# Kernel tuning notes

Hardware: AMD Instinct MI355X
Metric: run time of the kernel (lower is better)

## Reference

```python
import jax, jax.numpy as jnp
import numpy as np

B, L, C, H, W = 2, 3, 64, 32, 32
DI, N, DT_RANK, K = 128, 16, 4, 4  # d_inner=2*C, d_state, dt_rank=ceil(C/16), 4 scan dirs


def setup_inputs() -> dict:
    key = jax.random.key(0)
    ks = iter(jax.random.split(key, 48))
    nrm = lambda shape, s=0.02: jax.random.normal(next(ks), shape, jnp.float32) * s
    return {
        "image_sequence": jax.random.normal(next(ks), (B, L, C, H, W), jnp.float32),
        "difficult_zone": jax.random.normal(next(ks), (B, C, H, W), jnp.float32),
        "sigma": jax.random.uniform(next(ks), (B, C, H, W), jnp.float32),
        # LayerNorm2d applied to each frame
        "norm_g": jnp.ones((C,)), "norm_b": jnp.zeros((C,)),
        # ConvolutionalResBlock (in=3C -> out=C), GroupNorm(num_groups=1)
        "gn1_g": jnp.ones((3 * C,)), "gn1_b": jnp.zeros((3 * C,)),
        "conv1_w": nrm((C, 3 * C, 3, 3)), "conv1_b": jnp.zeros((C,)),
        "gn2_g": jnp.ones((C,)), "gn2_b": jnp.zeros((C,)),
        "conv2_w": nrm((C, C, 3, 3)), "conv2_b": jnp.zeros((C,)),
        "skip_w": nrm((C, 3 * C, 1, 1)), "skip_b": jnp.zeros((C,)),
        # VSSBlock pre-norms
        "ln1_g": jnp.ones((C,)), "ln1_b": jnp.zeros((C,)),
        "ln2_g": jnp.ones((C,)), "ln2_b": jnp.zeros((C,)),
        # SS2D
        "in_proj_w": nrm((2 * DI, C)),
        "dwconv_w": nrm((DI, 1, 3, 3)), "dwconv_b": jnp.zeros((DI,)),
        "x_proj_w": nrm((K, DT_RANK + 2 * N, DI)),
        "dt_proj_w": nrm((K, DI, DT_RANK), 0.1),
        "dt_proj_b": jnp.log(jnp.expm1(jnp.full((K, DI), 0.01, jnp.float32))),
        "A_logs": jnp.log(jnp.tile(jnp.arange(1, N + 1, dtype=jnp.float32), (K * DI, 1))),
        "Ds": jnp.ones((K * DI,)),
        "out_norm_g": jnp.ones((DI,)), "out_norm_b": jnp.zeros((DI,)),
        "out_proj_w": nrm((C, DI)),
        # Mlp (hidden = C)
        "fc1_w": nrm((C, C)), "fc1_b": jnp.zeros((C,)),
        "fc2_w": nrm((C, C)), "fc2_b": jnp.zeros((C,)),
    }


def _ln(x, g, b, eps=1e-5):  # layernorm over last axis
    m = x.mean(-1, keepdims=True)
    v = x.var(-1, keepdims=True)
    return (x - m) * jax.lax.rsqrt(v + eps) * g + b


def _ln2d(x, g, b, eps=1e-6):  # per-pixel channel layernorm, NCHW
    m = x.mean(1, keepdims=True)
    v = x.var(1, keepdims=True)
    return (x - m) * jax.lax.rsqrt(v + eps) * g[None, :, None, None] + b[None, :, None, None]


def _gn1(x, g, b, eps=1e-5):  # GroupNorm(num_groups=1), NCHW
    m = x.mean((1, 2, 3), keepdims=True)
    v = x.var((1, 2, 3), keepdims=True)
    return (x - m) * jax.lax.rsqrt(v + eps) * g[None, :, None, None] + b[None, :, None, None]


def _conv(x, w, b, pad):
    y = jax.lax.conv_general_dilated(x, w, (1, 1), [(pad, pad), (pad, pad)],
                                     dimension_numbers=("NCHW", "OIHW", "NCHW"))
    return y + b[None, :, None, None]


def _forward(image_sequence, difficult_zone, sigma, norm_g, norm_b, gn1_g, gn1_b,
             conv1_w, conv1_b, gn2_g, gn2_b, conv2_w, conv2_b, skip_w, skip_b,
             ln1_g, ln1_b, ln2_g, ln2_b, in_proj_w, dwconv_w, dwconv_b, x_proj_w,
             dt_proj_w, dt_proj_b, A_logs, Ds, out_norm_g, out_norm_b, out_proj_w,
             fc1_w, fc1_b, fc2_w, fc2_b):
    b, l, c, h, w = image_sequence.shape
    bl, L2 = b * l, h * w
    # fold frame loop into batch (identical math per frame in the torch loop)
    frames = _ln2d(image_sequence.reshape(bl, c, h, w), norm_g, norm_b)
    dz = jnp.broadcast_to(difficult_zone[:, None], (b, l, c, h, w)).reshape(bl, c, h, w)
    sg = jnp.broadcast_to(sigma[:, None], (b, l, c, h, w)).reshape(bl, c, h, w)
    x = jnp.concatenate([dz, frames, sg], axis=1)  # [bl, 3c, h, w]
    # channel compressor: pre-act conv res block
    hdn = _conv(jax.nn.silu(_gn1(x, gn1_g, gn1_b)), conv1_w, conv1_b, 1)
    hdn = _conv(jax.nn.silu(_gn1(hdn, gn2_g, gn2_b)), conv2_w, conv2_b, 1)
    x = hdn + _conv(x, skip_w, skip_b, 0)          # [bl, c, h, w]
    x = x.transpose(0, 2, 3, 1)                    # [bl, h, w, c]
    # --- VSSBlock (pre-norm): x = x + SS2D(LN(x)) ---
    xn = _ln(x, ln1_g, ln1_b)
    xz = xn @ in_proj_w.T                          # [bl,h,w,2*DI]
    xc, z = jnp.split(xz, 2, axis=-1)
    xc = xc.transpose(0, 3, 1, 2)                  # [bl, DI, h, w]
    xc = jax.lax.conv_general_dilated(xc, dwconv_w, (1, 1), [(1, 1), (1, 1)],
                                      dimension_numbers=("NCHW", "OIHW", "NCHW"),
                                      feature_group_count=DI) + dwconv_b[None, :, None, None]
    xc = jax.nn.silu(xc)
    # 4-direction scan inputs (HW, WH, and their reverses)
    xf = xc.reshape(bl, DI, L2)
    xt = xc.transpose(0, 1, 3, 2).reshape(bl, DI, L2)
    xs = jnp.stack([xf, xt], axis=1)
    xs = jnp.concatenate([xs, jnp.flip(xs, axis=-1)], axis=1)  # [bl, 4, DI, L2]
    x_dbl = jnp.einsum("bkdl,kcd->bkcl", xs, x_proj_w)
    dts, Bs, Cs = jnp.split(x_dbl, [DT_RANK, DT_RANK + N], axis=2)
    dts = jnp.einsum("bkrl,kdr->bkdl", dts, dt_proj_w) + dt_proj_b[None, :, :, None]
    dts = jax.nn.softplus(dts)                     # [bl, 4, DI, L2]
    A = -jnp.exp(A_logs).reshape(K, DI, N)
    dA = jnp.exp(dts[..., None] * A[None, :, :, None, :])            # [bl,4,DI,L2,N]
    dBu = dts[..., None] * Bs.transpose(0, 1, 3, 2)[:, :, None] * xs[..., None]
    a_t = dA.transpose(3, 0, 1, 2, 4)              # [L2, bl, 4, DI, N]
    bu_t = dBu.transpose(3, 0, 1, 2, 4)
    c_t = Cs.transpose(3, 0, 1, 2)                 # [L2, bl, 4, N]

    def step(hid, inp):
        a_i, bu_i, c_i = inp
        hid = a_i * hid + bu_i
        return hid, jnp.einsum("bkdn,bkn->bkd", hid, c_i)

    h0 = jnp.zeros((bl, K, DI, N), xs.dtype)
    _, ys = jax.lax.scan(step, h0, (a_t, bu_t, c_t))                 # [L2, bl, 4, DI]
    ys = ys.transpose(1, 2, 3, 0) + xs * Ds.reshape(K, DI)[None, :, :, None]
    inv = jnp.flip(ys[:, 2:4], axis=-1)
    y = (ys[:, 0] + inv[:, 0]
         + ys[:, 1].reshape(bl, DI, w, h).transpose(0, 1, 3, 2).reshape(bl, DI, L2)
         + inv[:, 1].reshape(bl, DI, w, h).transpose(0, 1, 3, 2).reshape(bl, DI, L2))
    y = _ln(y.transpose(0, 2, 1), out_norm_g, out_norm_b).reshape(bl, h, w, DI)
    y = y * jax.nn.silu(z)
    x = x + y @ out_proj_w.T
    # --- x = x + Mlp(LN(x)) ---
    xn = _ln(x, ln2_g, ln2_b)
    x = x + (jax.nn.gelu(xn @ fc1_w.T + fc1_b, approximate=False) @ fc2_w.T + fc2_b)
    return x.transpose(0, 3, 1, 2).reshape(b, l, c, h, w)


def reference(image_sequence, difficult_zone, sigma, norm_g, norm_b, gn1_g, gn1_b,
              conv1_w, conv1_b, gn2_g, gn2_b, conv2_w, conv2_b, skip_w, skip_b,
              ln1_g, ln1_b, ln2_g, ln2_b, in_proj_w, dwconv_w, dwconv_b, x_proj_w,
              dt_proj_w, dt_proj_b, A_logs, Ds, out_norm_g, out_norm_b, out_proj_w,
              fc1_w, fc1_b, fc2_w, fc2_b):
    return _forward(image_sequence, difficult_zone, sigma, norm_g, norm_b, gn1_g, gn1_b,
                    conv1_w, conv1_b, gn2_g, gn2_b, conv2_w, conv2_b, skip_w, skip_b,
                    ln1_g, ln1_b, ln2_g, ln2_b, in_proj_w, dwconv_w, dwconv_b, x_proj_w,
                    dt_proj_w, dt_proj_b, A_logs, Ds, out_norm_g, out_norm_b, out_proj_w,
                    fc1_w, fc1_b, fc2_w, fc2_b)
```

## Files before the change

### kernel.cpp

```cpp
#include <hip/hip_runtime.h>
#include <math.h>

#define BL    6
#define CCH   64
#define C3    192
#define L2    1024
#define DIC   128
#define NST   16
#define K4    4
#define PSTR  1088
#define NCH   32

#define LOG2E 1.44269504088896340736f
#define LN2C  0.69314718055994530942f

__device__ __forceinline__ float fexp(float x){ return __builtin_amdgcn_exp2f(x*LOG2E); }
__device__ __forceinline__ float fsilu(float x){ return x * __builtin_amdgcn_rcpf(1.f + fexp(-x)); }
__device__ __forceinline__ float fsoftplus(float x){
  if (x > 20.f) return x;
  return __builtin_amdgcn_logf(1.f + fexp(x)) * LN2C;
}
__device__ __forceinline__ float fgelu(float x){
  return 0.5f*x*(1.f + erff(x*0.70710678118654752440f));
}

__global__ __launch_bounds__(256) void k_ln2d(const float* __restrict__ img,
    const float* __restrict__ dz, const float* __restrict__ sg,
    const float* __restrict__ g, const float* __restrict__ b, float* __restrict__ x3c,
    float* __restrict__ psum1, float* __restrict__ psq1){
  __shared__ float ps[4][8], pq[4][8], gs[4], gq[4];
  int s = blockIdx.x >> 7;
  int pg = blockIdx.x & 127;
  int tid = threadIdx.x;
  int px = tid & 7; int cg = tid >> 3;
  int wv = tid >> 6; int lane = tid & 63;
  int p = pg*8 + px;
  int bsmp = s/3;
  const float* fr = img + (size_t)s*CCH*L2;
  float vals[2]; float sm=0.f, sq=0.f;
  #pragma unroll
  for (int j=0;j<2;++j){
    int c = cg*2 + j;
    float v = fr[c*L2 + p];
    vals[j]=v; sm+=v; sq+=v*v;
  }
  sm += __shfl_xor(sm,8,64);  sq += __shfl_xor(sq,8,64);
  sm += __shfl_xor(sm,16,64); sq += __shfl_xor(sq,16,64);
// ... 27 lines not shown
    psq1 [blockIdx.x] = gq[0]+gq[1]+gq[2]+gq[3];
  }
}

__global__ __launch_bounds__(256) void k_gnact1_skip(const float* __restrict__ x3c,
    const float* __restrict__ psum, const float* __restrict__ psq,
    const float* __restrict__ g, const float* __restrict__ b,
    const float* __restrict__ wsk,
    float* __restrict__ xact1, float* __restrict__ part){
  int bx = blockIdx.x;
  int tid = threadIdx.x;
  if (bx < 1152){
    int s = bx / C3; int c = bx % C3;
    float sm=0.f, sq=0.f;
    for (int i=0;i<128;++i){ sm += psum[s*128+i]; sq += psq[s*128+i]; }
    float mean = sm*(1.f/(C3*L2));
    float var = sq*(1.f/(C3*L2)) - mean*mean;
    float rs = rsqrtf(var + 1e-5f);
    float gc = g[c]*rs; float bc = b[c] - mean*rs*g[c];
    float4 v = *(const float4*)(x3c + (size_t)bx*1024 + tid*4);
    float4 o; o.x = fsilu(v.x*gc+bc); o.y = fsilu(v.y*gc+bc);
    o.z = fsilu(v.z*gc+bc); o.w = fsilu(v.w*gc+bc);
    float* pl = xact1 + (size_t)bx*PSTR;
    *(float4*)(pl + 32 + tid*4) = o;
    float4 z4 = make_float4(0.f,0.f,0.f,0.f);
    if (tid < 8)  *(float4*)(pl + tid*4) = z4;
    else if (tid < 16) *(float4*)(pl + 1056 + (tid-8)*4) = z4;
  } else {
    int t = bx - 1152;
    int role = t & 1; int cop = (t>>1)&31; int s = t >> 6;
    int co0 = cop*2, co1 = co0+1;
    int row = tid>>3; int q = tid&7; int col0 = q*4;
    int p = row*32+col0;
    float4 a0 = make_float4(0.f,0.f,0.f,0.f);
    float4 a1 = make_float4(0.f,0.f,0.f,0.f);
    int ci0 = role*96;
    const float* x3 = x3c + ((size_t)s*C3 + ci0)*L2 + p;
    const float* w0p = wsk + co0*C3 + ci0;
    const float* w1p = wsk + co1*C3 + ci0;
    #pragma unroll 4
    for (int ci=0; ci<96; ++ci){
      float4 v = *(const float4*)(x3 + (size_t)ci*L2);
      float ws0 = w0p[ci], ws1 = w1p[ci];
      a0.x = fmaf(ws0,v.x,a0.x); a0.y = fmaf(ws0,v.y,a0.y); a0.z = fmaf(ws0,v.z,a0.z); a0.w = fmaf(ws0,v.w,a0.w);
      a1.x = fmaf(ws1,v.x,a1.x); a1.y = fmaf(ws1,v.y,a1.y); a1.z = fmaf(ws1,v.z,a1.z); a1.w = fmaf(ws1,v.w,a1.w);
    }
    float* pp = part + (size_t)(4+role)*(BL*CCH*L2) + ((size_t)s*CCH+co0)*L2 + p;
    *(float4*)pp = a0;
    *(float4*)(pp+L2) = a1;
  }
}

__global__ __launch_bounds__(256) void k_gnact_pad(const float* __restrict__ x,
    const float* __restrict__ psum, const float* __restrict__ psq,
    const float* __restrict__ g, const float* __restrict__ b,
    int ch, int parts, float inv_n, float eps, float* __restrict__ out){
  int bx = blockIdx.x;
  int s = bx / ch; int c = bx % ch;
  int tid = threadIdx.x;
  float sm=0.f, sq=0.f;
  for (int i=0;i<parts;++i){ sm += psum[s*parts+i]; sq += psq[s*parts+i]; }
  float mean = sm*inv_n;
  float var = sq*inv_n - mean*mean;
  float rs = rsqrtf(var + eps);
  float gc = g[c]*rs; float bc = b[c] - mean*rs*g[c];
  float4 v = *(const float4*)(x + (size_t)bx*1024 + tid*4);
  float4 o; o.x = fsilu(v.x*gc+bc); o.y = fsilu(v.y*gc+bc);
  o.z = fsilu(v.z*gc+bc); o.w = fsilu(v.w*gc+bc);
  float* pl = out + (size_t)bx*PSTR;
  *(float4*)(pl + 32 + tid*4) = o;
  float4 z4 = make_float4(0.f,0.f,0.f,0.f);
  if (tid < 8)  *(float4*)(pl + tid*4) = z4;
  else if (tid < 16) *(float4*)(pl + 1056 + (tid-8)*4) = z4;
}

__device__ __forceinline__ void conv_row_acc(float4& a0, float4& a1, float4 mid, float lf, float rt,
    const float* wp0, const float* wp1){
  float w0=wp0[0], w1=wp0[1], w2=wp0[2];
  a0.x = fmaf(w0,lf,   fmaf(w1,mid.x, fmaf(w2,mid.y, a0.x)));
  a0.y = fmaf(w0,mid.x,fmaf(w1,mid.y, fmaf(w2,mid.z, a0.y)));
  a0.z = fmaf(w0,mid.y,fmaf(w1,mid.z, fmaf(w2,mid.w, a0.z)));
  a0.w = fmaf(w0,mid.z,fmaf(w1,mid.w, fmaf(w2,rt,    a0.w)));
  float v0=wp1[0], v1=wp1[1], v2=wp1[2];
  a1.x = fmaf(v0,lf,   fmaf(v1,mid.x, fmaf(v2,mid.y, a1.x)));
  a1.y = fmaf(v0,mid.x,fmaf(v1,mid.y, fmaf(v2,mid.z, a1.y)));
  a1.z = fmaf(v0,mid.y,fmaf(v1,mid.z, fmaf(v2,mid.w, a1.z)));
  a1.w = fmaf(v0,mid.z,fmaf(v1,mid.w, fmaf(v2,rt,    a1.w)));
}

__device__ __forceinline__ void conv_ci_body(float4 m0, float4 m1, float4 m2, int q,
    const float* wp0, const float* wp1, float4& a0, float4& a1){
  float lf0=__shfl_up(m0.w,1,64), rt0=__shfl_down(m0.x,1,64);
  float lf1=__shfl_up(m1.w,1,64), rt1=__shfl_down(m1.x,1,64);
  float lf2=__shfl_up(m2.w,1,64), rt2=__shfl_down(m2.x,1,64);
  if (q==0){ lf0=0.f; lf1=0.f; lf2=0.f; }
  if (q==7){ rt0=0.f; rt1=0.f; rt2=0.f; }
  conv_row_acc(a0,a1,m0,lf0,rt0, wp0+0, wp1+0);
  conv_row_acc(a0,a1,m1,lf1,rt1, wp0+3, wp1+3);
  conv_row_acc(a0,a1,m2,lf2,rt2, wp0+6, wp1+6);
}

__global__ __launch_bounds__(256) void k_conv1_split(const float* __restrict__ xact,
    const float* __restrict__ w, float* __restrict__ part){
  int bx = blockIdx.x; int kk = bx % 12; int r = bx / 12;
  int cop = r & 31; int s = r >> 5;
  int co0 = cop*2, co1 = co0+1;
  int tid = threadIdx.x; int row = tid>>3; int q = tid&7; int col0 = q*4;
  float4 a0 = make_float4(0.f,0.f,0.f,0.f);
  float4 a1 = make_float4(0.f,0.f,0.f,0.f);
  int ci0 = kk*16;
  const float* pl = xact + ((size_t)s*C3 + ci0)*PSTR + row*32 + col0;
  const float* wp0 = w + (size_t)(co0*C3 + ci0)*9;
  const float* wp1 = w + (size_t)(co1*C3 + ci0)*9;
  float4 m0 = *(const float4*)(pl);
  float4 m1 = *(const float4*)(pl+32);
  float4 m2 = *(const float4*)(pl+64);
  #pragma unroll 2
  for (int i=0;i<16;++i){
    const float* pn = pl + (i<15 ? PSTR : 0);
    float4 n0 = *(const float4*)(pn);
    float4 n1 = *(const float4*)(pn+32);
    float4 n2 = *(const float4*)(pn+64);
    conv_ci_body(m0,m1,m2,q, wp0, wp1, a0, a1);
    wp0 += 9; wp1 += 9; pl = pn; m0=n0; m1=n1; m2=n2;
  }
  float* pp = part + (size_t)kk*(BL*CCH*L2) + ((size_t)s*CCH+co0)*L2 + row*32+col0;
  *(float4*)pp = a0;
  *(float4*)(pp+L2) = a1;
}

__global__ __launch_bounds__(256) void k_reduce1(const float* __restrict__ part,
    const float* __restrict__ bias, float* __restrict__ h1,
    float* __restrict__ psum2, float* __restrict__ psq2){
  int co = blockIdx.x & 63; int s = blockIdx.x >> 6;
  size_t ofs = ((size_t)s*CCH+co)*L2 + threadIdx.x*4;
  const size_t stride = (size_t)BL*CCH*L2;
  float4 acc = *(const float4*)(part + ofs);
  #pragma unroll
  for (int kk=1;kk<12;++kk){
    float4 r = *(const float4*)(part + (size_t)kk*stride + ofs);
    acc.x += r.x; acc.y += r.y; acc.z += r.z; acc.w += r.w;
  }
  float bv = bias[co];
  acc.x += bv; acc.y += bv; acc.z += bv; acc.w += bv;
  *(float4*)(h1 + ofs) = acc;
  float sm = acc.x+acc.y+acc.z+acc.w;
  float sq = acc.x*acc.x+acc.y*acc.y+acc.z*acc.z+acc.w*acc.w;
  for (int m=1;m<64;m<<=1){ sm+=__shfl_xor(sm,m,64); sq+=__shfl_xor(sq,m,64); }
  __shared__ float s_sm[4], s_sq[4];
  int wv = threadIdx.x>>6;
  if ((threadIdx.x&63)==0){ s_sm[wv]=sm; s_sq[wv]=sq; }
  __syncthreads();
  if (threadIdx.x==0){
    psum2[blockIdx.x] = s_sm[0]+s_sm[1]+s_sm[2]+s_sm[3];
    psq2 [blockIdx.x] = s_sq[0]+s_sq[1]+s_sq[2]+s_sq[3];
  }
}

__global__ __launch_bounds__(256) void k_conv2_split(const float* __restrict__ xact2,
    const float* __restrict__ w2, float* __restrict__ part){
  int bx = blockIdx.x; int role = bx & 3; int t = bx >> 2;
  int cop = t & 31; int s = t >> 5;
  int co0 = cop*2, co1 = co0+1;
  int tid = threadIdx.x; int row = tid>>3; int q = tid&7; int col0 = q*4;
  int p = row*32+col0;
  float4 a0 = make_float4(0.f,0.f,0.f,0.f);
  float4 a1 = make_float4(0.f,0.f,0.f,0.f);
  int ci0 = role*16;
  const float* pl = xact2 + ((size_t)s*CCH + ci0)*PSTR + row*32 + col0;
  const float* wp0 = w2 + (size_t)(co0*CCH + ci0)*9;
  const float* wp1 = w2 + (size_t)(co1*CCH + ci0)*9;
  float4 m0 = *(const float4*)(pl);
  float4 m1 = *(const float4*)(pl+32);
  float4 m2 = *(const float4*)(pl+64);
  #pragma unroll 2
  for (int i=0;i<16;++i){
    const float* pn = pl + (i<15 ? PSTR : 0);
    float4 n0 = *(const float4*)(pn);
    float4 n1 = *(const float4*)(pn+32);
    float4 n2 = *(const float4*)(pn+64);
    conv_ci_body(m0,m1,m2,q, wp0, wp1, a0, a1);
    wp0 += 9; wp1 += 9; pl = pn; m0=n0; m1=n1; m2=n2;
  }
  float* pp = part + (size_t)role*(BL*CCH*L2) + ((size_t)s*CCH+co0)*L2 + p;
  *(float4*)pp = a0;
  *(float4*)(pp+L2) = a1;
}

__global__ __launch_bounds__(256) void k_red2_ln1_inproj(const float* __restrict__ part,
    const float* __restrict__ b2, const float* __restrict__ bsk,
    const float* __restrict__ g, const float* __restrict__ b,
    const float* __restrict__ W,
    float* __restrict__ x_cmaj, float* __restrict__ xc, float* __restrict__ z_t){
  __shared__ float xn_s[64*65];
  int bx = blockIdx.x; int oq = bx & 7; int pg = (bx>>3)&15; int s = bx>>7;
  int p0 = pg*64;
  int tid = threadIdx.x;
  const size_t stride = (size_t)BL*CCH*L2;
  #pragma unroll
  for (int kq=0;kq<4;++kq){
    int f = kq*256 + tid;
    int co = f >> 4; int px4 = (f & 15)*4;
    size_t ofs = ((size_t)s*CCH+co)*L2 + p0 + px4;
    float4 r0 = *(const float4*)(part + ofs);
    float4 r1 = *(const float4*)(part + stride + ofs);
    float4 r2 = *(const float4*)(part + 2*stride + ofs);
    float4 r3 = *(const float4*)(part + 3*stride + ofs);
    float4 r4 = *(const float4*)(part + 4*stride + ofs);
    float4 r5 = *(const float4*)(part + 5*stride + ofs);
    float bv = b2[co]+bsk[co];
    float4 o;
    o.x = ((r0.x+r1.x)+(r2.x+r3.x))+(r4.x+r5.x)+bv;
    o.y = ((r0.y+r1.y)+(r2.y+r3.y))+(r4.y+r5.y)+bv;
    o.z = ((r0.z+r1.z)+(r2.z+r3.z))+(r4.z+r5.z)+bv;
    o.w = ((r0.w+r1.w)+(r2.w+r3.w))+(r4.w+r5.w)+bv;
    if (oq == 0) *(float4*)(x_cmaj + ofs) = o;
    xn_s[(px4+0)*65 + co] = o.x;
    xn_s[(px4+1)*65 + co] = o.y;
    xn_s[(px4+2)*65 + co] = o.z;
    xn_s[(px4+3)*65 + co] = o.w;
  }
  __syncthreads();
  {
    int wv = __builtin_amdgcn_readfirstlane(tid>>6); int lane = tid&63;
    for (int j=0;j<16;++j){
      int pl = wv*16 + j;
      float v = xn_s[pl*65 + lane];
      float sm = v, sq = v*v;
      for (int m=1;m<64;m<<=1){ sm += __shfl_xor(sm,m,64); sq += __shfl_xor(sq,m,64); }
      float mean = sm*(1.f/64.f); float var = sq*(1.f/64.f) - mean*mean;
      float rs = rsqrtf(var + 1e-5f);
      xn_s[pl*65 + lane] = (v-mean)*rs*g[lane] + b[lane];
    }
  }
  __syncthreads();
  int px_l = tid & 63;
  int og = __builtin_amdgcn_readfirstlane(tid >> 6);
  int o0 = oq*32 + og*8;
  float acc[8];
  #pragma unroll
  for (int oi=0;oi<8;++oi) acc[oi]=0.f;
  for (int c=0;c<64;++c){
    float xv = xn_s[px_l*65 + c];
    #pragma unroll
    for (int oi=0;oi<8;++oi) acc[oi] = fmaf(W[(o0+oi)*64 + c], xv, acc[oi]);
  }
  int p = p0 + px_l;
  if (oq < 4){
    #pragma unroll
    for (int oi=0;oi<8;++oi) xc[((size_t)s*DIC + o0 + oi)*L2 + p] = acc[oi];
  } else {
    #pragma unroll
    for (int oi=0;oi<8;++oi) z_t[((size_t)s*DIC + (o0-128) + oi)*L2 + p] = acc[oi];
  }
}

__global__ __launch_bounds__(256) void k_xproj_dt(const float* __restrict__ xc,
    const float* __restrict__ dww, const float* __restrict__ dwb,
    const float* __restrict__ W,
    float* __restrict__ dtr, float* __restrict__ Bp, float* __restrict__ Cp,
    float* __restrict__ u_t){
  __shared__ float smem[128*68];
  int bx = blockIdx.x; int pg = bx & 15; int sk = bx >> 4;
  int k = sk & 3; int s = sk >> 2;
  int tid = threadIdx.x;
  for (int i = tid; i < 128*16; i += 256){
    int dr = i>>4; int j4 = (i&15)*4;
    int rw = j4>>5; int col0 = j4 & 31;
    int gr = pg*2 + rw;
    int q = i&7;
    const float* xr = xc + ((size_t)s*DIC+dr)*L2;
    const float* wp = dww + dr*9;
    float bv = dwb[dr];
    float4 acc = make_float4(bv,bv,bv,bv);
    #pragma unroll
    for (int dy=-1;dy<=1;++dy){
      int r = gr+dy;
      float4 mid = make_float4(0.f,0.f,0.f,0.f);
      if (0<=r && r<32) mid = *(const float4*)(xr + r*32 + col0);
      float lf = __shfl_up(mid.w,1,64); if(q==0) lf=0.f;
      float rt = __shfl_down(mid.x,1,64); if(q==7) rt=0.f;
      float w0=wp[(dy+1)*3], w1=wp[(dy+1)*3+1], w2=wp[(dy+1)*3+2];
      acc.x = fmaf(w0,lf,   fmaf(w1,mid.x, fmaf(w2,mid.y, acc.x)));
      acc.y = fmaf(w0,mid.x,fmaf(w1,mid.y, fmaf(w2,mid.z, acc.y)));
      acc.z = fmaf(w0,mid.y,fmaf(w1,mid.z, fmaf(w2,mid.w, acc.z)));
      acc.w = fmaf(w0,mid.z,fmaf(w1,mid.w, fmaf(w2,rt,    acc.w)));
    }
    acc.x = fsilu(acc.x); acc.y = fsilu(acc.y); acc.z = fsilu(acc.z); acc.w = fsilu(acc.w);
    *(float4*)&smem[dr*68 + j4] = acc;
  }
  __syncthreads();
  if (k == 0){
    float* ub = u_t + ((size_t)(s*L2) + pg*64)*DIC;
    for (int i = tid; i < 64*128; i += 256){
      int px2 = i>>7; int dd = i&127;
      ub[(size_t)px2*DIC + dd] = smem[dd*68 + px2];
    }
  }
  int px = tid & 63;
  int cgrp = __builtin_amdgcn_readfirstlane(tid >> 6);
  int c0 = cgrp*9;
  const float* wb = W + (size_t)(k*36 + c0)*DIC;
  float acc[9];
  #pragma unroll
  for (int ci=0;ci<9;++ci) acc[ci]=0.f;
  for (int d=0; d<DIC; ++d){
    float xv = smem[d*68 + px];
    #pragma unroll
    for (int ci=0;ci<9;++ci) acc[ci] = fmaf(wb[ci*DIC+d], xv, acc[ci]);
  }
  __syncthreads();
  #pragma unroll
  for (int ci=0;ci<9;++ci) smem[(c0+ci)*68 + px] = acc[ci];
  __syncthreads();
  {
    int pp = tid >> 2; int r = tid & 3;
    dtr[((size_t)sk*L2 + pg*64 + pp)*4 + r] = smem[r*68 + pp];
  }
  float* Bb = Bp + ((size_t)sk*L2 + pg*64)*NST;
  float* Cb = Cp + ((size_t)sk*L2 + pg*64)*NST;
  for (int i = tid; i < 1024; i += 256){
    int pp = i>>4; int n = i&15;
    Bb[pp*NST + n] = smem[(4+n)*68 + pp];
    Cb[pp*NST + n] = smem[(20+n)*68 + pp];
  }
}

__device__ __forceinline__ int scan_pix32(int ch, int j, int k){
  if (k==0) return ch*32 + j;
  if (k==1) return j*32 + ch;
  if (k==2) return 1023 - (ch*32 + j);
  return 1023 - (j*32 + ch);
}

struct StepH { float4 dt4; float uv; float4 B0,B1; };
__device__ __forceinline__ StepH loadH(const float* dr, const float* ub, const float* Bb, int p){
  StepH r;
  r.dt4 = *(const float4*)(dr + (size_t)p*4);
  r.uv = ub[(size_t)p*DIC];
  const float* bp = Bb + p*NST;
  r.B0 = *(const float4*)bp; r.B1 = *(const float4*)(bp+4);
  return r;
}
__device__ __forceinline__ float dt_eval(float4 w4, float bb, float4 d4){
  return fsoftplus(fmaf(w4.x,d4.x,fmaf(w4.y,d4.y,fmaf(w4.z,d4.z,fmaf(w4.w,d4.w,bb)))));
}

__global__ __launch_bounds__(256,4) void k_scan_part3(const float* __restrict__ dtr,
    const float* __restrict__ dtw, const float* __restrict__ dtb,
    const float* __restrict__ u_t, const float* __restrict__ Bp,
    const float* __restrict__ A_logs, float* __restrict__ hend, float* __restrict__ Ssum){
  int bx = blockIdx.x; int ch = bx & 31; int sk = bx >> 5;
  int k = sk & 3; int s = sk >> 2;
  int tid = threadIdx.x; int d = tid >> 1; int nh = tid & 1;
  float aco[8];
  {
    const float* ab = A_logs + (size_t)(k*DIC+d)*NST + nh*8;
    #pragma unroll
    for (int n=0;n<8;++n) aco[n] = -LOG2E * fexp(ab[n]);
  }
  float4 w4 = *(const float4*)(dtw + (size_t)(k*DIC+d)*4);
  float bb = dtb[k*DIC+d];
  float h[8]; float Sacc = 0.f;
  #pragma unroll
  for (int n=0;n<8;++n) h[n]=0.f;
  const float* dr = dtr + (size_t)sk*L2*4;
  const float* ub = u_t + (size_t)s*L2*DIC + d;
  const float* Bb = Bp + (size_t)sk*L2*NST + nh*8;
  StepH cur = loadH(dr, ub, Bb, scan_pix32(ch, 0, k));
  #pragma unroll 4
  for (int j=0;j<32;++j){
    StepH nxt;
    if (j < 31) nxt = loadH(dr, ub, Bb, scan_pix32(ch, j+1, k));
    float dtv = dt_eval(w4, bb, cur.dt4);
    Sacc += dtv;
    float tv = dtv*cur.uv;
    #define PSTEP(NI, BV) { float a_ = __builtin_amdgcn_exp2f(dtv*aco[NI]); \
      h[NI] = fmaf(a_, h[NI], tv*(BV)); }
    PSTEP(0,cur.B0.x) PSTEP(1,cur.B0.y) PSTEP(2,cur.B0.z) PSTEP(3,cur.B0.w)
    PSTEP(4,cur.B1.x) PSTEP(5,cur.B1.y) PSTEP(6,cur.B1.z) PSTEP(7,cur.B1.w)
    #undef PSTEP
    cur = nxt;
  }
  size_t base = ((size_t)(sk*NCH + ch)*DIC + d)*NST + nh*8;
  *(float4*)(hend + base)     = make_float4(h[0],h[1],h[2],h[3]);
  *(float4*)(hend + base + 4) = make_float4(h[4],h[5],h[6],h[7]);
  if (nh == 0) Ssum[(size_t)(sk*NCH + ch)*DIC + d] = Sacc;
}

__global__ __launch_bounds__(256) void k_scan_fix3(const float* __restrict__ hend,
    const float* __restrict__ Ssum, const float* __restrict__ A_logs,
    float* __restrict__ Hin){
  int t = blockIdx.x*256 + threadIdx.x;
  int n = t & 15; int d = (t>>4) & 127; int sk = t >> 11; int k = sk & 3;
  float aco = -LOG2E * fexp(A_logs[(size_t)(k*DIC+d)*NST + n]);
  float H = 0.f;
  #pragma unroll 8
  for (int ch=0; ch<NCH; ++ch){
    size_t sidx = (size_t)(sk*NCH + ch)*DIC + d;
    float pa = __builtin_amdgcn_exp2f(aco * Ssum[sidx]);
    float he = hend[sidx*NST + n];
    Hin[sidx*NST + n] = H;
    H = fmaf(pa, H, he);
  }
}

__global__ __launch_bounds__(256,4) void k_scan_y3(const float* __restrict__ dtr,
    const float* __restrict__ dtw, const float* __restrict__ dtb,
    const float* __restrict__ u_t, const float* __restrict__ Bp, const float* __restrict__ Cp,
    const float* __restrict__ A_logs, const float* __restrict__ Ds,
    const float* __restrict__ Hin, float* __restrict__ ys_t){
  int bx = blockIdx.x; int ch = bx & 31; int sk = bx >> 5;
  int k = sk & 3; int s = sk >> 2;
  int tid = threadIdx.x; int d = tid >> 1; int nh = tid & 1;
  float aco[8];
  {
    const float* ab = A_logs + (size_t)(k*DIC+d)*NST + nh*8;
    #pragma unroll
    for (int n=0;n<8;++n) aco[n] = -LOG2E * fexp(ab[n]);
  }
  float4 w4 = *(const float4*)(dtw + (size_t)(k*DIC+d)*4);
  float bb = dtb[k*DIC+d];
  float Dv = Ds[k*DIC+d];
  float h[8];
  size_t hbase = ((size_t)(sk*NCH + ch)*DIC + d)*NST + nh*8;
  {
    float4 h0 = *(const float4*)(Hin + hbase);
    float4 h1 = *(const float4*)(Hin + hbase + 4);
    h[0]=h0.x; h[1]=h0.y; h[2]=h0.z; h[3]=h0.w;
    h[4]=h1.x; h[5]=h1.y; h[6]=h1.z; h[7]=h1.w;
  }
  const float* dr = dtr + (size_t)sk*L2*4;
  const float* ub = u_t + (size_t)s*L2*DIC + d;
  const float* Bb = Bp + (size_t)sk*L2*NST + nh*8;
  const float* Cb = Cp + (size_t)sk*L2*NST + nh*8;
  float* yb = ys_t + (size_t)sk*L2*DIC + d;
  int pcur = scan_pix32(ch, 0, k);
  StepH cur = loadH(dr, ub, Bb, pcur);
  float4 Cc0 = *(const float4*)(Cb + pcur*NST);
  float4 Cc1 = *(const float4*)(Cb + pcur*NST + 4);
  #pragma unroll 4
  for (int j=0;j<32;++j){
    StepH nxt; float4 Cn0, Cn1; int pn = pcur;
    if (j < 31){
      pn = scan_pix32(ch, j+1, k);
      nxt = loadH(dr, ub, Bb, pn);
      Cn0 = *(const float4*)(Cb + pn*NST);
      Cn1 = *(const float4*)(Cb + pn*NST + 4);
    }
    float dtv = dt_eval(w4, bb, cur.dt4);
    float tv = dtv*cur.uv;
    float y0=0.f, y1=0.f, y2=0.f, y3=0.f;
    #define YSTEP(NI, BV, CV, YA) { float a_ = __builtin_amdgcn_exp2f(dtv*aco[NI]); \
      h[NI] = fmaf(a_, h[NI], tv*(BV)); YA = fmaf(h[NI], (CV), YA); }
    YSTEP(0,cur.B0.x,Cc0.x,y0) YSTEP(1,cur.B0.y,Cc0.y,y1) YSTEP(2,cur.B0.z,Cc0.z,y2) YSTEP(3,cur.B0.w,Cc0.w,y3)
    YSTEP(4,cur.B1.x,Cc1.x,y0) YSTEP(5,cur.B1.y,Cc1.y,y1) YSTEP(6,cur.B1.z,Cc1.z,y2) YSTEP(7,cur.B1.w,Cc1.w,y3)
    #undef YSTEP
    float py = (y0+y1)+(y2+y3);
    float tot = py + __shfl_xor(py, 1, 64);
    if (nh == 0) yb[(size_t)pcur*DIC] = fmaf(cur.uv, Dv, tot);
    cur = nxt; Cc0 = Cn0; Cc1 = Cn1; pcur = pn;
  }
}

__global__ __launch_bounds__(256) void k_tail(const float* __restrict__ ys_t,
    const float* __restrict__ z_t, const float* __restrict__ ong, const float* __restrict__ onb,
    const float* __restrict__ Wop, const float* __restrict__ x_cmaj,
    const float* __restrict__ g2, const float* __restrict__ b2n,
    const float* __restrict__ w1, const float* __restrict__ b1,
    const float* __restrict__ w2, const float* __restrict__ b2,
    float* __restrict__ out){
  __shared__ float yt[128*9];
  __shared__ float xvt[64*9];
  __shared__ float ts[64*9];
  int s = blockIdx.x >> 7; int pg = blockIdx.x & 127;
  int tid = threadIdx.x;
  {
    int wv = __builtin_amdgcn_readfirstlane(tid>>6); int lane = tid&63;
    int d0 = lane, d1 = lane+64;
    for (int i=0;i<2;++i){
      int px = i*4 + wv; int p = pg*8 + px;
      const float* yb = ys_t + ((size_t)(s*4)*L2 + p)*DIC;
      float ya = yb[d0] + yb[(size_t)L2*DIC + d0] + yb[(size_t)2*L2*DIC + d0] + yb[(size_t)3*L2*DIC + d0];
      float yc = yb[d1] + yb[(size_t)L2*DIC + d1] + yb[(size_t)2*L2*DIC + d1] + yb[(size_t)3*L2*DIC + d1];
      float sm = ya+yc, sq = ya*ya+yc*yc;
      for (int m=1;m<64;m<<=1){ sm+=__shfl_xor(sm,m,64); sq+=__shfl_xor(sq,m,64); }
      float mean = sm*(1.f/128.f); float var = sq*(1.f/128.f)-mean*mean;
      float rs = rsqrtf(var + 1e-5f);
      float yn0 = (ya-mean)*rs*ong[d0] + onb[d0];
      float yn1 = (yc-mean)*rs*ong[d1] + onb[d1];
      float zv0 = z_t[((size_t)s*DIC+d0)*L2 + p];
      float zv1 = z_t[((size_t)s*DIC+d1)*L2 + p];
      yt[d0*9 + px] = yn0 * fsilu(zv0);
      yt[d1*9 + px] = yn1 * fsilu(zv1);
    }
  }
  __syncthreads();
  {
    int px = tid & 7; int cgp = tid >> 3;
    int c0 = cgp*2;
    float a0=0.f,a1=0.f;
    for (int d=0; d<DIC; ++d){
      float yv = yt[d*9 + px];
      a0 = fmaf(Wop[(c0+0)*DIC + d], yv, a0);
      a1 = fmaf(Wop[(c0+1)*DIC + d], yv, a1);
    }
    int p = pg*8 + px;
    size_t base = ((size_t)s*CCH + c0)*L2 + p;
    xvt[(c0+0)*9 + px] = x_cmaj[base]    + a0;
    xvt[(c0+1)*9 + px] = x_cmaj[base+L2] + a1;
  }
  __syncthreads();
  int px = tid & 7; int cgp = tid >> 3;
  float sm=0.f, sq=0.f;
  for (int c=0;c<64;++c){ float v = xvt[c*9+px]; sm+=v; sq+=v*v; }
  float mean = sm*(1.f/64.f);
  float rs = rsqrtf(sq*(1.f/64.f) - mean*mean + 1e-5f);
  int o0 = cgp*2;
  float t0 = b1[o0], t1 = b1[o0+1];
  for (int c=0;c<64;++c){
    float xn = (xvt[c*9+px]-mean)*rs*g2[c] + b2n[c];
    t0 = fmaf(xn, w1[(o0+0)*64 + c], t0);
    t1 = fmaf(xn, w1[(o0+1)*64 + c], t1);
  }
  ts[(o0+0)*9 + px] = fgelu(t0);
  ts[(o0+1)*9 + px] = fgelu(t1);
  __syncthreads();
  int c0 = cgp*2;
  float acc0 = xvt[(c0+0)*9+px] + b2[c0+0];
  float acc1 = xvt[(c0+1)*9+px] + b2[c0+1];
  for (int o=0;o<64;++o){
    float tv = ts[o*9+px];
    acc0 = fmaf(tv, w2[(c0+0)*64 + o], acc0);
    acc1 = fmaf(tv, w2[(c0+1)*64 + o], acc1);
  }
  int p = pg*8 + px;
  out[((size_t)s*CCH + c0+0)*L2 + p] = acc0;
  out[((size_t)s*CCH + c0+1)*L2 + p] = acc1;
}

extern "C" void kernel_launch(void* const* d_in, const int* in_sizes, int n_in,
                              void* d_out, int out_size, void* d_ws, size_t ws_size,
                              hipStream_t stream){
  (void)in_sizes; (void)n_in; (void)out_size; (void)ws_size;
  const float* img      = (const float*)d_in[0];
  const float* dz       = (const float*)d_in[1];
  const float* sg       = (const float*)d_in[2];
  const float* norm_g   = (const float*)d_in[3];
  const float* norm_b   = (const float*)d_in[4];
  const float* gn1_g    = (const float*)d_in[5];
  const float* gn1_b    = (const float*)d_in[6];
  const float* conv1_w  = (const float*)d_in[7];
  const float* conv1_b  = (const float*)d_in[8];
  const float* gn2_g    = (const float*)d_in[9];
  const float* gn2_b    = (const float*)d_in[10];
  const float* conv2_w  = (const float*)d_in[11];
  const float* conv2_b  = (const float*)d_in[12];
  const float* skip_w   = (const float*)d_in[13];
  const float* skip_b   = (const float*)d_in[14];
  const float* ln1_g    = (const float*)d_in[15];
  const float* ln1_b    = (const float*)d_in[16];
  const float* ln2_g    = (const float*)d_in[17];
  const float* ln2_b    = (const float*)d_in[18];
  const float* in_proj_w= (const float*)d_in[19];
  const float* dwconv_w = (const float*)d_in[20];
  const float* dwconv_b = (const float*)d_in[21];
  const float* x_proj_w = (const float*)d_in[22];
  const float* dt_proj_w= (const float*)d_in[23];
  const float* dt_proj_b= (const float*)d_in[24];
  const float* A_logs   = (const float*)d_in[25];
  const float* Ds       = (const float*)d_in[26];
// ... 54 lines not shown
```

Before: 286.7 us.

## Use packed FP32 FMAs and geometric decay recurrence in selective scan

Convolution, projection and MLP inner loops now accumulate through two-wide float vectors, so the compiler can emit packed FP32 FMA instructions (v_pk_fma_f32) that do two output channels per instruction. The scan kernels also check at runtime whether A equals n times A0, as it does for the log(arange) initialisation. When it does, the eight per-state exp2 calls are replaced by two exp2 calls plus a chain of multiplies. The check keeps the general path for any other A, but the multiply chain adds rounding error and a serial dependency, and packed FMAs can require extra register moves.

```diff
diff --git a/kernel.cpp b/kernel.cpp
--- a/kernel.cpp
+++ b/kernel.cpp
@@ -13,6 +13,13 @@
 
 #define LOG2E 1.44269504088896340736f
 #define LN2C  0.69314718055994530942f
+
+typedef float f2 __attribute__((ext_vector_type(2)));
+__device__ __forceinline__ f2 mkf2(float a, float b){ f2 r; r.x=a; r.y=b; return r; }
+__device__ __forceinline__ f2 fma2(f2 a, float b, f2 c){
+  f2 bb; bb.x=b; bb.y=b;
+  return __builtin_elementwise_fma(a, bb, c);
+}
 
 __device__ __forceinline__ float fexp(float x){ return __builtin_amdgcn_exp2f(x*LOG2E); }
 __device__ __forceinline__ float fsilu(float x){ return x * __builtin_amdgcn_rcpf(1.f + fexp(-x)); }
@@ -106,8 +113,9 @@
     int co0 = cop*2, co1 = co0+1;
     int row = tid>>3; int q = tid&7; int col0 = q*4;
     int p = row*32+col0;
-    float4 a0 = make_float4(0.f,0.f,0.f,0.f);
-    float4 a1 = make_float4(0.f,0.f,0.f,0.f);
+    f2 a[4];
+    #pragma unroll
+    for (int i=0;i<4;++i){ a[i].x=0.f; a[i].y=0.f; }
     int ci0 = role*96;
     const float* x3 = x3c + ((size_t)s*C3 + ci0)*L2 + p;
     const float* w0p = wsk + co0*C3 + ci0;
@@ -115,13 +123,15 @@
     #pragma unroll 4
     for (int ci=0; ci<96; ++ci){
       float4 v = *(const float4*)(x3 + (size_t)ci*L2);
-      float ws0 = w0p[ci], ws1 = w1p[ci];
-      a0.x = fmaf(ws0,v.x,a0.x); a0.y = fmaf(ws0,v.y,a0.y); a0.z = fmaf(ws0,v.z,a0.z); a0.w = fmaf(ws0,v.w,a0.w);
-      a1.x = fmaf(ws1,v.x,a1.x); a1.y = fmaf(ws1,v.y,a1.y); a1.z = fmaf(ws1,v.z,a1.z); a1.w = fmaf(ws1,v.w,a1.w);
+      f2 w = mkf2(w0p[ci], w1p[ci]);
+      a[0] = fma2(w, v.x, a[0]);
+      a[1] = fma2(w, v.y, a[1]);
+      a[2] = fma2(w, v.z, a[2]);
+      a[3] = fma2(w, v.w, a[3]);
     }
     float* pp = part + (size_t)(4+role)*(BL*CCH*L2) + ((size_t)s*CCH+co0)*L2 + p;
-    *(float4*)pp = a0;
-    *(float4*)(pp+L2) = a1;
+    *(float4*)pp = make_float4(a[0].x,a[1].x,a[2].x,a[3].x);
+    *(float4*)(pp+L2) = make_float4(a[0].y,a[1].y,a[2].y,a[3].y);
   }
 }
 
@@ -148,30 +158,27 @@
   else if (tid < 16) *(float4*)(pl + 1056 + (tid-8)*4) = z4;
 }
 
-__device__ __forceinline__ void conv_row_acc(float4& a0, float4& a1, float4 mid, float lf, float rt,
+__device__ __forceinline__ void conv_row_acc2(f2* a, float4 mid, float lf, float rt,
     const float* wp0, const float* wp1){
-  float w0=wp0[0], w1=wp0[1], w2=wp0[2];
-  a0.x = fmaf(w0,lf,   fmaf(w1,mid.x, fmaf(w2,mid.y, a0.x)));
-  a0.y = fmaf(w0,mid.x,fmaf(w1,mid.y, fmaf(w2,mid.z, a0.y)));
-  a0.z = fmaf(w0,mid.y,fmaf(w1,mid.z, fmaf(w2,mid.w, a0.z)));
-  a0.w = fmaf(w0,mid.z,fmaf(w1,mid.w, fmaf(w2,rt,    a0.w)));
-  float v0=wp1[0], v1=wp1[1], v2=wp1[2];
-  a1.x = fmaf(v0,lf,   fmaf(v1,mid.x, fmaf(v2,mid.y, a1.x)));
-  a1.y = fmaf(v0,mid.x,fmaf(v1,mid.y, fmaf(v2,mid.z, a1.y)));
-  a1.z = fmaf(v0,mid.y,fmaf(v1,mid.z, fmaf(v2,mid.w, a1.z)));
-  a1.w = fmaf(v0,mid.z,fmaf(v1,mid.w, fmaf(v2,rt,    a1.w)));
-}
-
-__device__ __forceinline__ void conv_ci_body(float4 m0, float4 m1, float4 m2, int q,
-    const float* wp0, const float* wp1, float4& a0, float4& a1){
+  f2 w0 = mkf2(wp0[0],wp1[0]);
+  f2 w1 = mkf2(wp0[1],wp1[1]);
+  f2 w2 = mkf2(wp0[2],wp1[2]);
+  a[0] = fma2(w0,lf,   fma2(w1,mid.x, fma2(w2,mid.y, a[0])));
+  a[1] = fma2(w0,mid.x,fma2(w1,mid.y, fma2(w2,mid.z, a[1])));
+  a[2] = fma2(w0,mid.y,fma2(w1,mid.z, fma2(w2,mid.w, a[2])));
+  a[3] = fma2(w0,mid.z,fma2(w1,mid.w, fma2(w2,rt,    a[3])));
+}
+
+__device__ __forceinline__ void conv_ci_body2(float4 m0, float4 m1, float4 m2, int q,
+    const float* wp0, const float* wp1, f2* a){
   float lf0=__shfl_up(m0.w,1,64), rt0=__shfl_down(m0.x,1,64);
   float lf1=__shfl_up(m1.w,1,64), rt1=__shfl_down(m1.x,1,64);
   float lf2=__shfl_up(m2.w,1,64), rt2=__shfl_down(m2.x,1,64);
   if (q==0){ lf0=0.f; lf1=0.f; lf2=0.f; }
   if (q==7){ rt0=0.f; rt1=0.f; rt2=0.f; }
-  conv_row_acc(a0,a1,m0,lf0,rt0, wp0+0, wp1+0);
-  conv_row_acc(a0,a1,m1,lf1,rt1, wp0+3, wp1+3);
-  conv_row_acc(a0,a1,m2,lf2,rt2, wp0+6, wp1+6);
+  conv_row_acc2(a,m0,lf0,rt0, wp0+0, wp1+0);
+  conv_row_acc2(a,m1,lf1,rt1, wp0+3, wp1+3);
+  conv_row_acc2(a,m2,lf2,rt2, wp0+6, wp1+6);
 }
 
 __global__ __launch_bounds__(256) void k_conv1_split(const float* __restrict__ xact,
@@ -180,8 +187,9 @@
   int cop = r & 31; int s = r >> 5;
   int co0 = cop*2, co1 = co0+1;
   int tid = threadIdx.x; int row = tid>>3; int q = tid&7; int col0 = q*4;
-  float4 a0 = make_float4(0.f,0.f,0.f,0.f);
-  float4 a1 = make_float4(0.f,0.f,0.f,0.f);
+  f2 a[4];
+  #pragma unroll
+  for (int i=0;i<4;++i){ a[i].x=0.f; a[i].y=0.f; }
   int ci0 = kk*16;
   const float* pl = xact + ((size_t)s*C3 + ci0)*PSTR + row*32 + col0;
   const float* wp0 = w + (size_t)(co0*C3 + ci0)*9;
@@ -195,12 +203,12 @@
     float4 n0 = *(const float4*)(pn);
     float4 n1 = *(const float4*)(pn+32);
     float4 n2 = *(const float4*)(pn+64);
-    conv_ci_body(m0,m1,m2,q, wp0, wp1, a0, a1);
+    conv_ci_body2(m0,m1,m2,q, wp0, wp1, a);
     wp0 += 9; wp1 += 9; pl = pn; m0=n0; m1=n1; m2=n2;
   }
   float* pp = part + (size_t)kk*(BL*CCH*L2) + ((size_t)s*CCH+co0)*L2 + row*32+col0;
-  *(float4*)pp = a0;
-  *(float4*)(pp+L2) = a1;
+  *(float4*)pp = make_float4(a[0].x,a[1].x,a[2].x,a[3].x);
+  *(float4*)(pp+L2) = make_float4(a[0].y,a[1].y,a[2].y,a[3].y);
 }
 
 __global__ __launch_bounds__(256) void k_reduce1(const float* __restrict__ part,
@@ -238,8 +246,9 @@
   int co0 = cop*2, co1 = co0+1;
   int tid = threadIdx.x; int row = tid>>3; int q = tid&7; int col0 = q*4;
   int p = row*32+col0;
-  float4 a0 = make_float4(0.f,0.f,0.f,0.f);
-  float4 a1 = make_float4(0.f,0.f,0.f,0.f);
+  f2 a[4];
+  #pragma unroll
+  for (int i=0;i<4;++i){ a[i].x=0.f; a[i].y=0.f; }
   int ci0 = role*16;
   const float* pl = xact2 + ((size_t)s*CCH + ci0)*PSTR + row*32 + col0;
   const float* wp0 = w2 + (size_t)(co0*CCH + ci0)*9;
@@ -253,12 +262,12 @@
     float4 n0 = *(const float4*)(pn);
     float4 n1 = *(const float4*)(pn+32);
     float4 n2 = *(const float4*)(pn+64);
-    conv_ci_body(m0,m1,m2,q, wp0, wp1, a0, a1);
+    conv_ci_body2(m0,m1,m2,q, wp0, wp1, a);
     wp0 += 9; wp1 += 9; pl = pn; m0=n0; m1=n1; m2=n2;
   }
   float* pp = part + (size_t)role*(BL*CCH*L2) + ((size_t)s*CCH+co0)*L2 + p;
-  *(float4*)pp = a0;
-  *(float4*)(pp+L2) = a1;
+  *(float4*)pp = make_float4(a[0].x,a[1].x,a[2].x,a[3].x);
+  *(float4*)(pp+L2) = make_float4(a[0].y,a[1].y,a[2].y,a[3].y);
 }
 
 __global__ __launch_bounds__(256) void k_red2_ln1_inproj(const float* __restrict__ part,
@@ -311,21 +320,28 @@
   int px_l = tid & 63;
   int og = __builtin_amdgcn_readfirstlane(tid >> 6);
   int o0 = oq*32 + og*8;
-  float acc[8];
-  #pragma unroll
-  for (int oi=0;oi<8;++oi) acc[oi]=0.f;
+  f2 acc[4];
+  #pragma unroll
+  for (int oi=0;oi<4;++oi){ acc[oi].x=0.f; acc[oi].y=0.f; }
   for (int c=0;c<64;++c){
     float xv = xn_s[px_l*65 + c];
     #pragma unroll
-    for (int oi=0;oi<8;++oi) acc[oi] = fmaf(W[(o0+oi)*64 + c], xv, acc[oi]);
+    for (int oi=0;oi<4;++oi)
+      acc[oi] = fma2(mkf2(W[(o0+2*oi)*64 + c], W[(o0+2*oi+1)*64 + c]), xv, acc[oi]);
   }
   int p = p0 + px_l;
   if (oq < 4){
     #pragma unroll
-    for (int oi=0;oi<8;++oi) xc[((size_t)s*DIC + o0 + oi)*L2 + p] = acc[oi];
+    for (int oi=0;oi<4;++oi){
+      xc[((size_t)s*DIC + o0 + 2*oi)*L2 + p]   = acc[oi].x;
+      xc[((size_t)s*DIC + o0 + 2*oi+1)*L2 + p] = acc[oi].y;
+    }
   } else {
     #pragma unroll
-    for (int oi=0;oi<8;++oi) z_t[((size_t)s*DIC + (o0-128) + oi)*L2 + p] = acc[oi];
+    for (int oi=0;oi<4;++oi){
+      z_t[((size_t)s*DIC + (o0-128) + 2*oi)*L2 + p]   = acc[oi].x;
+      z_t[((size_t)s*DIC + (o0-128) + 2*oi+1)*L2 + p] = acc[oi].y;
+    }
   }
 }
 
@@ -375,17 +391,23 @@
   int cgrp = __builtin_amdgcn_readfirstlane(tid >> 6);
   int c0 = cgrp*9;
   const float* wb = W + (size_t)(k*36 + c0)*DIC;
-  float acc[9];
-  #pragma unroll
-  for (int ci=0;ci<9;++ci) acc[ci]=0.f;
+  f2 acc2[4]; float acc8 = 0.f;
+  #pragma unroll
+  for (int ci=0;ci<4;++ci){ acc2[ci].x=0.f; acc2[ci].y=0.f; }
   for (int d=0; d<DIC; ++d){
     float xv = smem[d*68 + px];
     #pragma unroll
-    for (int ci=0;ci<9;++ci) acc[ci] = fmaf(wb[ci*DIC+d], xv, acc[ci]);
-  }
-  __syncthreads();
-  #pragma unroll
-  for (int ci=0;ci<9;++ci) smem[(c0+ci)*68 + px] = acc[ci];
+    for (int ci=0;ci<4;++ci)
+      acc2[ci] = fma2(mkf2(wb[(2*ci)*DIC+d], wb[(2*ci+1)*DIC+d]), xv, acc2[ci]);
+    acc8 = fmaf(wb[8*DIC+d], xv, acc8);
+  }
+  __syncthreads();
+  #pragma unroll
+  for (int ci=0;ci<4;++ci){
+    smem[(c0+2*ci)*68 + px]   = acc2[ci].x;
+    smem[(c0+2*ci+1)*68 + px] = acc2[ci].y;
+  }
+  smem[(c0+8)*68 + px] = acc8;
   __syncthreads();
   {
     int pp = tid >> 2; int r = tid & 3;
@@ -420,6 +442,16 @@
   return fsoftplus(fmaf(w4.x,d4.x,fmaf(w4.y,d4.y,fmaf(w4.z,d4.z,fmaf(w4.w,d4.w,bb)))));
 }
 
+__device__ __forceinline__ bool aco_linear(const float* aco, float acoR, int gbase){
+  bool ok = true;
+  #pragma unroll
+  for (int n=0;n<8;++n){
+    float ideal = (float)(gbase+n+1) * acoR;
+    ok = ok && (fabsf(aco[n]-ideal) <= 1e-5f*fabsf(ideal) + 1e-12f);
+  }
+  return ok;
+}
+
 __global__ __launch_bounds__(256,4) void k_scan_part3(const float* __restrict__ dtr,
     const float* __restrict__ dtw, const float* __restrict__ dtb,
     const float* __restrict__ u_t, const float* __restrict__ Bp,
@@ -428,11 +460,14 @@
   int k = sk & 3; int s = sk >> 2;
   int tid = threadIdx.x; int d = tid >> 1; int nh = tid & 1;
   float aco[8];
+  float acoR = -LOG2E * fexp(A_logs[(size_t)(k*DIC+d)*NST]);
   {
     const float* ab = A_logs + (size_t)(k*DIC+d)*NST + nh*8;
     #pragma unroll
     for (int n=0;n<8;++n) aco[n] = -LOG2E * fexp(ab[n]);
   }
+  bool fast = aco_linear(aco, acoR, nh*8);
+  float aco0 = aco[0];
   float4 w4 = *(const float4*)(dtw + (size_t)(k*DIC+d)*4);
   float bb = dtb[k*DIC+d];
   float h[8]; float Sacc = 0.f;
@@ -442,19 +477,41 @@
   const float* ub = u_t + (size_t)s*L2*DIC + d;
   const float* Bb = Bp + (size_t)sk*L2*NST + nh*8;
   StepH cur = loadH(dr, ub, Bb, scan_pix32(ch, 0, k));
-  #pragma unroll 4
-  for (int j=0;j<32;++j){
-    StepH nxt;
-    if (j < 31) nxt = loadH(dr, ub, Bb, scan_pix32(ch, j+1, k));
-    float dtv = dt_eval(w4, bb, cur.dt4);
-    Sacc += dtv;
-    float tv = dtv*cur.uv;
-    #define PSTEP(NI, BV) { float a_ = __builtin_amdgcn_exp2f(dtv*aco[NI]); \
-      h[NI] = fmaf(a_, h[NI], tv*(BV)); }
-    PSTEP(0,cur.B0.x) PSTEP(1,cur.B0.y) PSTEP(2,cur.B0.z) PSTEP(3,cur.B0.w)
-    PSTEP(4,cur.B1.x) PSTEP(5,cur.B1.y) PSTEP(6,cur.B1.z) PSTEP(7,cur.B1.w)
-    #undef PSTEP
-    cur = nxt;
+  if (fast){
+    #pragma unroll 4
+    for (int j=0;j<32;++j){
+      StepH nxt;
+      if (j < 31) nxt = loadH(dr, ub, Bb, scan_pix32(ch, j+1, k));
+      float dtv = dt_eval(w4, bb, cur.dt4);
+      Sacc += dtv;
+      float tv = dtv*cur.uv;
+      float rr = __builtin_amdgcn_exp2f(dtv*acoR);
+      float a_ = __builtin_amdgcn_exp2f(dtv*aco0);
+      h[0] = fmaf(a_, h[0], tv*cur.B0.x);
+      a_ *= rr; h[1] = fmaf(a_, h[1], tv*cur.B0.y);
+      a_ *= rr; h[2] = fmaf(a_, h[2], tv*cur.B0.z);
+      a_ *= rr; h[3] = fmaf(a_, h[3], tv*cur.B0.w);
+      a_ *= rr; h[4] = fmaf(a_, h[4], tv*cur.B1.x);
+      a_ *= rr; h[5] = fmaf(a_, h[5], tv*cur.B1.y);
+      a_ *= rr; h[6] = fmaf(a_, h[6], tv*cur.B1.z);
+      a_ *= rr; h[7] = fmaf(a_, h[7], tv*cur.B1.w);
+      cur = nxt;
+    }
+  } else {
+    #pragma unroll 4
+    for (int j=0;j<32;++j){
+      StepH nxt;
+      if (j < 31) nxt = loadH(dr, ub, Bb, scan_pix32(ch, j+1, k));
+      float dtv = dt_eval(w4, bb, cur.dt4);
+      Sacc += dtv;
+      float tv = dtv*cur.uv;
+      #define PSTEP(NI, BV) { float a_ = __builtin_amdgcn_exp2f(dtv*aco[NI]); \
+        h[NI] = fmaf(a_, h[NI], tv*(BV)); }
+      PSTEP(0,cur.B0.x) PSTEP(1,cur.B0.y) PSTEP(2,cur.B0.z) PSTEP(3,cur.B0.w)
+      PSTEP(4,cur.B1.x) PSTEP(5,cur.B1.y) PSTEP(6,cur.B1.z) PSTEP(7,cur.B1.w)
+      #undef PSTEP
+      cur = nxt;
+    }
   }
   size_t base = ((size_t)(sk*NCH + ch)*DIC + d)*NST + nh*8;
   *(float4*)(hend + base)     = make_float4(h[0],h[1],h[2],h[3]);
@@ -488,11 +545,14 @@
   int k = sk & 3; int s = sk >> 2;
   int tid = threadIdx.x; int d = tid >> 1; int nh = tid & 1;
   float aco[8];
+  float acoR = -LOG2E * fexp(A_logs[(size_t)(k*DIC+d)*NST]);
   {
     const float* ab = A_logs + (size_t)(k*DIC+d)*NST + nh*8;
     #pragma unroll
     for (int n=0;n<8;++n) aco[n] = -LOG2E * fexp(ab[n]);
   }
+  bool fast = aco_linear(aco, acoR, nh*8);
+  float aco0 = aco[0];
   float4 w4 = *(const float4*)(dtw + (size_t)(k*DIC+d)*4);
   float bb = dtb[k*DIC+d];
   float Dv = Ds[k*DIC+d];
@@ -513,27 +573,57 @@
   StepH cur = loadH(dr, ub, Bb, pcur);
   float4 Cc0 = *(const float4*)(Cb + pcur*NST);
   float4 Cc1 = *(const float4*)(Cb + pcur*NST + 4);
-  #pragma unroll 4
-  for (int j=0;j<32;++j){
-    StepH nxt; float4 Cn0, Cn1; int pn = pcur;
-    if (j < 31){
-      pn = scan_pix32(ch, j+1, k);
-      nxt = loadH(dr, ub, Bb, pn);
-      Cn0 = *(const float4*)(Cb + pn*NST);
-      Cn1 = *(const float4*)(Cb + pn*NST + 4);
-    }
-    float dtv = dt_eval(w4, bb, cur.dt4);
-    float tv = dtv*cur.uv;
-    float y0=0.f, y1=0.f, y2=0.f, y3=0.f;
-    #define YSTEP(NI, BV, CV, YA) { float a_ = __builtin_amdgcn_exp2f(dtv*aco[NI]); \
-      h[NI] = fmaf(a_, h[NI], tv*(BV)); YA = fmaf(h[NI], (CV), YA); }
-    YSTEP(0,cur.B0.x,Cc0.x,y0) YSTEP(1,cur.B0.y,Cc0.y,y1) YSTEP(2,cur.B0.z,Cc0.z,y2) YSTEP(3,cur.B0.w,Cc0.w,y3)
-    YSTEP(4,cur.B1.x,Cc1.x,y0) YSTEP(5,cur.B1.y,Cc1.y,y1) YSTEP(6,cur.B1.z,Cc1.z,y2) YSTEP(7,cur.B1.w,Cc1.w,y3)
-    #undef YSTEP
-    float py = (y0+y1)+(y2+y3);
-    float tot = py + __shfl_xor(py, 1, 64);
-    if (nh == 0) yb[(size_t)pcur*DIC] = fmaf(cur.uv, Dv, tot);
-    cur = nxt; Cc0 = Cn0; Cc1 = Cn1; pcur = pn;
+  if (fast){
+    #pragma unroll 4
+    for (int j=0;j<32;++j){
+      StepH nxt; float4 Cn0, Cn1; int pn = pcur;
+      if (j < 31){
+        pn = scan_pix32(ch, j+1, k);
+        nxt = loadH(dr, ub, Bb, pn);
+        Cn0 = *(const float4*)(Cb + pn*NST);
+        Cn1 = *(const float4*)(Cb + pn*NST + 4);
+      }
+      float dtv = dt_eval(w4, bb, cur.dt4);
+      float tv = dtv*cur.uv;
+      float y0=0.f, y1=0.f, y2=0.f, y3=0.f;
+      float rr = __builtin_amdgcn_exp2f(dtv*acoR);
+      float a_ = __builtin_amdgcn_exp2f(dtv*aco0);
+      h[0] = fmaf(a_, h[0], tv*cur.B0.x); y0 = fmaf(h[0], Cc0.x, y0);
+      a_ *= rr; h[1] = fmaf(a_, h[1], tv*cur.B0.y); y1 = fmaf(h[1], Cc0.y, y1);
+      a_ *= rr; h[2] = fmaf(a_, h[2], tv*cur.B0.z); y2 = fmaf(h[2], Cc0.z, y2);
+      a_ *= rr; h[3] = fmaf(a_, h[3], tv*cur.B0.w); y3 = fmaf(h[3], Cc0.w, y3);
+      a_ *= rr; h[4] = fmaf(a_, h[4], tv*cur.B1.x); y0 = fmaf(h[4], Cc1.x, y0);
+      a_ *= rr; h[5] = fmaf(a_, h[5], tv*cur.B1.y); y1 = fmaf(h[5], Cc1.y, y1);
+      a_ *= rr; h[6] = fmaf(a_, h[6], tv*cur.B1.z); y2 = fmaf(h[6], Cc1.z, y2);
+      a_ *= rr; h[7] = fmaf(a_, h[7], tv*cur.B1.w); y3 = fmaf(h[7], Cc1.w, y3);
+      float py = (y0+y1)+(y2+y3);
+      float tot = py + __shfl_xor(py, 1, 64);
+      if (nh == 0) yb[(size_t)pcur*DIC] = fmaf(cur.uv, Dv, tot);
+      cur = nxt; Cc0 = Cn0; Cc1 = Cn1; pcur = pn;
+    }
+  } else {
+    #pragma unroll 4
+    for (int j=0;j<32;++j){
+      StepH nxt; float4 Cn0, Cn1; int pn = pcur;
+      if (j < 31){
+        pn = scan_pix32(ch, j+1, k);
+        nxt = loadH(dr, ub, Bb, pn);
+        Cn0 = *(const float4*)(Cb + pn*NST);
+        Cn1 = *(const float4*)(Cb + pn*NST + 4);
+      }
+      float dtv = dt_eval(w4, bb, cur.dt4);
+      float tv = dtv*cur.uv;
+      float y0=0.f, y1=0.f, y2=0.f, y3=0.f;
+      #define YSTEP(NI, BV, CV, YA) { float a_ = __builtin_amdgcn_exp2f(dtv*aco[NI]); \
+        h[NI] = fmaf(a_, h[NI], tv*(BV)); YA = fmaf(h[NI], (CV), YA); }
+      YSTEP(0,cur.B0.x,Cc0.x,y0) YSTEP(1,cur.B0.y,Cc0.y,y1) YSTEP(2,cur.B0.z,Cc0.z,y2) YSTEP(3,cur.B0.w,Cc0.w,y3)
+      YSTEP(4,cur.B1.x,Cc1.x,y0) YSTEP(5,cur.B1.y,Cc1.y,y1) YSTEP(6,cur.B1.z,Cc1.z,y2) YSTEP(7,cur.B1.w,Cc1.w,y3)
+      #undef YSTEP
+      float py = (y0+y1)+(y2+y3);
+      float tot = py + __shfl_xor(py, 1, 64);
+      if (nh == 0) yb[(size_t)pcur*DIC] = fmaf(cur.uv, Dv, tot);
+      cur = nxt; Cc0 = Cn0; Cc1 = Cn1; pcur = pn;
+    }
   }
 }
 
@@ -573,16 +663,15 @@
   {
     int px = tid & 7; int cgp = tid >> 3;
     int c0 = cgp*2;
-    float a0=0.f,a1=0.f;
+    f2 A; A.x=0.f; A.y=0.f;
     for (int d=0; d<DIC; ++d){
       float yv = yt[d*9 + px];
-      a0 = fmaf(Wop[(c0+0)*DIC + d], yv, a0);
-      a1 = fmaf(Wop[(c0+1)*DIC + d], yv, a1);
+      A = fma2(mkf2(Wop[(c0+0)*DIC + d], Wop[(c0+1)*DIC + d]), yv, A);
     }
     int p = pg*8 + px;
     size_t base = ((size_t)s*CCH + c0)*L2 + p;
-    xvt[(c0+0)*9 + px] = x_cmaj[base]    + a0;
-    xvt[(c0+1)*9 + px] = x_cmaj[base+L2] + a1;
+    xvt[(c0+0)*9 + px] = x_cmaj[base]    + A.x;
+    xvt[(c0+1)*9 + px] = x_cmaj[base+L2] + A.y;
   }
   __syncthreads();
   int px = tid & 7; int cgp = tid >> 3;
@@ -591,26 +680,23 @@
   float mean = sm*(1.f/64.f);
   float rs = rsqrtf(sq*(1.f/64.f) - mean*mean + 1e-5f);
   int o0 = cgp*2;
-  float t0 = b1[o0], t1 = b1[o0+1];
+  f2 T = mkf2(b1[o0], b1[o0+1]);
   for (int c=0;c<64;++c){
     float xn = (xvt[c*9+px]-mean)*rs*g2[c] + b2n[c];
-    t0 = fmaf(xn, w1[(o0+0)*64 + c], t0);
-    t1 = fmaf(xn, w1[(o0+1)*64 + c], t1);
-  }
-  ts[(o0+0)*9 + px] = fgelu(t0);
-  ts[(o0+1)*9 + px] = fgelu(t1);
+    T = fma2(mkf2(w1[(o0+0)*64 + c], w1[(o0+1)*64 + c]), xn, T);
+  }
+  ts[(o0+0)*9 + px] = fgelu(T.x);
+  ts[(o0+1)*9 + px] = fgelu(T.y);
   __syncthreads();
   int c0 = cgp*2;
-  float acc0 = xvt[(c0+0)*9+px] + b2[c0+0];
-  float acc1 = xvt[(c0+1)*9+px] + b2[c0+1];
+  f2 ACC = mkf2(xvt[(c0+0)*9+px] + b2[c0+0], xvt[(c0+1)*9+px] + b2[c0+1]);
   for (int o=0;o<64;++o){
     float tv = ts[o*9+px];
-    acc0 = fmaf(tv, w2[(c0+0)*64 + o], acc0);
-    acc1 = fmaf(tv, w2[(c0+1)*64 + o], acc1);
+    ACC = fma2(mkf2(w2[(c0+0)*64 + o], w2[(c0+1)*64 + o]), tv, ACC);
   }
   int p = pg*8 + px;
-  out[((size_t)s*CCH + c0+0)*L2 + p] = acc0;
-  out[((size_t)s*CCH + c0+1)*L2 + p] = acc1;
+  out[((size_t)s*CCH + c0+0)*L2 + p] = ACC.x;
+  out[((size_t)s*CCH + c0+1)*L2 + p] = ACC.y;
 }
 
 extern "C" void kernel_launch(void* const* d_in, const int* in_sizes, int n_in,
```

After: 286.4 us. About the same (-0.1%).
